# Optimization experiments

Measured on AMD Instinct MI355X. Metric: run time of the kernel, lower is better.

Reference implementation:

```python
import jax, jax.numpy as jnp
import numpy as np

N, E, F_IN, H, C = 50000, 800000, 64, 4, 32
NEG_SLOPE = 0.2  # PyG GATConv default negative_slope
LN_EPS = 1e-5


def setup_inputs() -> dict:
    key = jax.random.key(0)
    ks = jax.random.split(key, 8)
    s = 1.0 / np.sqrt(F_IN)
    return {
        "x": jax.random.normal(ks[0], (N, F_IN), jnp.float32),
        "edge_index": jax.random.randint(ks[1], (2, E), 0, N, jnp.int64),
        "W": jax.random.normal(ks[2], (F_IN, H * C), jnp.float32) * s,
        "att_src": jax.random.normal(ks[3], (H, C), jnp.float32) * s,
        "att_dst": jax.random.normal(ks[4], (H, C), jnp.float32) * s,
        "bias": jnp.zeros((H * C,), jnp.float32),
        "res_w": jax.random.normal(ks[5], (F_IN, H * C), jnp.float32) * s,
        "res_b": jnp.zeros((H * C,), jnp.float32),
        "ln_g": jnp.ones((H * C,), jnp.float32),
        "ln_b": jnp.zeros((H * C,), jnp.float32),
    }


def reference(x, edge_index, W, att_src, att_dst, bias, res_w, res_b, ln_g, ln_b):
    n = x.shape[0]
    # GATConv adds self-loops by default
    loop = jnp.arange(n, dtype=edge_index.dtype)
    src = jnp.concatenate([edge_index[0], loop])
    dst = jnp.concatenate([edge_index[1], loop])

    h = (x @ W).reshape(n, H, C)                      # [N,H,C]
    a_src = jnp.einsum('nhc,hc->nh', h, att_src)       # [N,H]
    a_dst = jnp.einsum('nhc,hc->nh', h, att_dst)

    e = a_src[src] + a_dst[dst]                        # [Etot,H]
    e = jnp.where(e >= 0, e, NEG_SLOPE * e)            # leaky_relu

    # segment softmax over destination nodes
    m = jax.ops.segment_max(e, dst, num_segments=n)    # [N,H]
    ex = jnp.exp(e - m[dst])
    denom = jax.ops.segment_sum(ex, dst, num_segments=n)
    alpha = ex / denom[dst]                            # [Etot,H]

    msg = h[src] * alpha[:, :, None]                   # [Etot,H,C]
    out = jax.ops.segment_sum(msg, dst, num_segments=n)  # [N,H,C]
    out = out.reshape(n, H * C) + bias

    # elu; dropout is identity in eval mode
    out = jnp.where(out > 0, out, jnp.expm1(out))
    out = out + (x @ res_w + res_b)                    # residual Linear

    mu = out.mean(-1, keepdims=True)
    var = ((out - mu) ** 2).mean(-1, keepdims=True)
    return ln_g * (out - mu) * jax.lax.rsqrt(var + LN_EPS) + ln_b
```

## Files before the change

### kernel.cpp

```cpp
#include <hip/hip_runtime.h>

#define F_IN 64
#define NH 4
#define HC 128
#define NEG_SLOPE 0.2f
#define LN_EPS 1e-5f
#define NC_CHUNK 128
#define BUCKET 128
#define KW_BLOCKS 64

typedef __bf16 bf16_8 __attribute__((ext_vector_type(8)));
typedef float  f32_4  __attribute__((ext_vector_type(4)));

__device__ inline int detect_is64(const int* __restrict__ ei, int E) {
    int lane = threadIdx.x & 63;
    long long stride = (2LL * E) / 65;
    int w = ei[(((long long)(lane + 1)) * stride) | 1];
    return __ballot(w != 0) == 0ULL;
}

__device__ inline unsigned bfpack(float a, float b) {
    unsigned ua = __float_as_uint(a), ub = __float_as_uint(b);
    ua = (ua + 0x7fffu + ((ua >> 16) & 1u)) >> 16;
    ub = (ub + 0x7fffu + ((ub >> 16) & 1u)) >> 16;
    return ua | (ub << 16);
}

__device__ inline float wave_bcast_sum(float v) {
#pragma unroll
    for (int off = 32; off > 0; off >>= 1) v += __shfl_down(v, off, 64);
    return __shfl(v, 0, 64);
}

__global__ __launch_bounds__(256) void k_prep(
    const float* __restrict__ W, const float* __restrict__ res_w,
    const int* __restrict__ ei, int E,
    __bf16* __restrict__ wt, int* __restrict__ counts, int NB, int chunk)
{
    if ((int)blockIdx.x < KW_BLOCKS) {
        int idx = blockIdx.x * 256 + threadIdx.x;
        int ch = idx >> 6, k = idx & 63;
        const float* src = (ch < HC) ? W : res_w;
        wt[ch * 64 + k] = (__bf16)src[k * HC + (ch & (HC - 1))];
        return;
    }
    __shared__ int cnt[512];
    int c = blockIdx.x - KW_BLOCKS;
    for (int i = threadIdx.x; i < NB; i += 256) cnt[i] = 0;
    __syncthreads();
    int is64 = detect_is64(ei, E);
    int base = c * chunk, end = min(E, base + chunk);
    for (int idx = base + threadIdx.x; idx < end; idx += 256) {
        int d = is64 ? ei[2 * (E + idx)] : ei[E + idx];
        atomicAdd(&cnt[d >> 7], 1);
    }
    __syncthreads();
    for (int b = threadIdx.x; b < NB; b += 256)
        counts[c * NB + b] = cnt[b];
}

__global__ __launch_bounds__(256) void k_main(
    const float* __restrict__ x, const __bf16* __restrict__ wt,
    const float* __restrict__ att_src, const float* __restrict__ att_dst,
    unsigned* __restrict__ h_bf, unsigned* __restrict__ r_bf,
    float* __restrict__ a_s, float* __restrict__ a_d, int n, int nka,
    const int* __restrict__ ei, int E, const int* __restrict__ counts,
    int* __restrict__ epacked, int* __restrict__ sbase_g, int NB, int chunk)
{
    __shared__ int cur[512];
    __shared__ int ss[256];

    if ((int)blockIdx.x < nka) {
        int tid = threadIdx.x;
        int wv_ = tid >> 6, lane = tid & 63;
        int col = lane & 15, quad = lane >> 4;
        int node = blockIdx.x * 64 + wv_ * 16 + col;
        int nrow = (node < n) ? node : (n - 1);

        bf16_8 bx0, bx1;
        {
            const float* xp = &x[nrow * F_IN + quad * 8];
            float4 p0 = *(const float4*)(xp);
            float4 p1 = *(const float4*)(xp + 4);
            float4 p2 = *(const float4*)(xp + 32);
            float4 p3 = *(const float4*)(xp + 36);
            bx0[0] = (__bf16)p0.x; bx0[1] = (__bf16)p0.y; bx0[2] = (__bf16)p0.z; bx0[3] = (__bf16)p0.w;
            bx0[4] = (__bf16)p1.x; bx0[5] = (__bf16)p1.y; bx0[6] = (__bf16)p1.z; bx0[7] = (__bf16)p1.w;
            bx1[0] = (__bf16)p2.x; bx1[1] = (__bf16)p2.y; bx1[2] = (__bf16)p2.z; bx1[3] = (__bf16)p2.w;
            bx1[4] = (__bf16)p3.x; bx1[5] = (__bf16)p3.y; bx1[6] = (__bf16)p3.z; bx1[7] = (__bf16)p3.w;
        }

        float vs[4] = {0.f, 0.f, 0.f, 0.f};
        float vd[4] = {0.f, 0.f, 0.f, 0.f};

#pragma unroll
        for (int mt = 0; mt < 16; ++mt) {
            const __bf16* ap = &wt[(mt * 16 + col) * 64 + quad * 8];
            bf16_8 a0 = *(const bf16_8*)ap;
            bf16_8 a1 = *(const bf16_8*)(ap + 32);
            f32_4 acc = {0.f, 0.f, 0.f, 0.f};
            acc = __builtin_amdgcn_mfma_f32_16x16x32_bf16(a0, bx0, acc, 0, 0, 0);
            acc = __builtin_amdgcn_mfma_f32_16x16x32_bf16(a1, bx1, acc, 0, 0, 0);
            int ch0 = mt * 16 + quad * 4;
            if (mt < 8) {
                float4 as4 = *(const float4*)&att_src[ch0];
                float4 ad4 = *(const float4*)&att_dst[ch0];
                int head = mt >> 1;
                vs[head] += acc[0] * as4.x + acc[1] * as4.y + acc[2] * as4.z + acc[3] * as4.w;
                vd[head] += acc[0] * ad4.x + acc[1] * ad4.y + acc[2] * ad4.z + acc[3] * ad4.w;
                if (node < n) {
                    uint2 pk = make_uint2(bfpack(acc[0], acc[1]), bfpack(acc[2], acc[3]));
                    *(uint2*)&h_bf[node * 64 + (ch0 >> 1)] = pk;
                }
            } else {
                if (node < n) {
                    uint2 pk = make_uint2(bfpack(acc[0], acc[1]), bfpack(acc[2], acc[3]));
                    *(uint2*)&r_bf[node * 64 + ((ch0 - 128) >> 1)] = pk;
                }
            }
        }

#pragma unroll
        for (int hh = 0; hh < NH; ++hh) {
            vs[hh] += __shfl_down(vs[hh], 32, 64);
            vs[hh] += __shfl_down(vs[hh], 16, 64);
            vd[hh] += __shfl_down(vd[hh], 32, 64);
            vd[hh] += __shfl_down(vd[hh], 16, 64);
        }
        if (quad == 0 && node < n) {
            *(float4*)&a_s[node * NH] = make_float4(vs[0], vs[1], vs[2], vs[3]);
            *(float4*)&a_d[node * NH] = make_float4(vd[0], vd[1], vd[2], vd[3]);
        }
        return;
    }

    int c = blockIdx.x - nka;
    int t = threadIdx.x;
    int b0 = 2 * t, b1 = 2 * t + 1;

    int f0 = 0, f1 = 0, p0 = 0, p1 = 0;
    for (int cc = 0; cc < NC_CHUNK; ++cc) {
        int v0 = (b0 < NB) ? counts[cc * NB + b0] : 0;
        int v1 = (b1 < NB) ? counts[cc * NB + b1] : 0;
        f0 += v0; f1 += v1;
        if (cc < c) { p0 += v0; p1 += v1; }
    }
    ss[t] = f0 + f1;
    __syncthreads();
#pragma unroll
    for (int off = 1; off < 256; off <<= 1) {
        int u = (t >= off) ? ss[t - off] : 0;
        __syncthreads();
        ss[t] += u;
        __syncthreads();
    }
    int ebase = ss[t] - (f0 + f1);
    int base0 = ebase;
    int base1 = ebase + f0;
    if (b0 < NB) cur[b0] = base0 + p0;
    if (b1 < NB) cur[b1] = base1 + p1;
    if (c == 0) {
        if (b0 <= NB) sbase_g[b0] = base0;
        if (b1 <= NB) sbase_g[b1] = base1;
    }
    __syncthreads();

    int is64 = detect_is64(ei, E);
    int base = c * chunk, end = min(E, base + chunk);
    for (int idx = base + t; idx < end; idx += 256) {
        int s = is64 ? ei[2 * idx] : ei[idx];
        int d = is64 ? ei[2 * (E + idx)] : ei[E + idx];
        int p = atomicAdd(&cur[d >> 7], 1);
        epacked[p] = ((d & (BUCKET - 1)) << 16) | s;
    }
}

__global__ __launch_bounds__(256) void kd_sort(
    const int* __restrict__ sbase_g, const int* __restrict__ epacked,
    int* __restrict__ sorted_src, int* __restrict__ offsets,
    int NB, int n, int E)
{
    __shared__ int hist[BUCKET];
    __shared__ int sc[BUCKET];
    __shared__ int cur[BUCKET];
    int b = blockIdx.x;
    int s0 = sbase_g[b];
    int s1 = sbase_g[b + 1];
    int t = threadIdx.x;
    if (t < BUCKET) hist[t] = 0;
    __syncthreads();
    for (int e = s0 + t; e < s1; e += 256)
        atomicAdd(&hist[((unsigned)epacked[e]) >> 16], 1);
    __syncthreads();
    if (t < BUCKET) sc[t] = hist[t];
    __syncthreads();
#pragma unroll
    for (int o = 1; o < BUCKET; o <<= 1) {
        int u = (t >= o && t < BUCKET) ? sc[t - o] : 0;
        __syncthreads();
        if (t < BUCKET) sc[t] += u;
        __syncthreads();
    }
    if (t < BUCKET) {
        int excl = sc[t] - hist[t];
        cur[t] = s0 + excl;
        int d = b * BUCKET + t;
        if (d < n) offsets[d] = s0 + excl;
    }
    if (b == NB - 1 && t == 0) offsets[n] = E;
    __syncthreads();
    for (int e = s0 + t; e < s1; e += 256) {
        int p = epacked[e];
        int pos = atomicAdd(&cur[((unsigned)p) >> 16], 1);
        sorted_src[pos] = p & 0xFFFF;
    }
}

__global__ __launch_bounds__(256) void k_agg(
    const int* __restrict__ offsets, const int* __restrict__ src_sorted,
    const float* __restrict__ a_s, const float* __restrict__ a_d,
    const unsigned int* __restrict__ h_bf, const unsigned int* __restrict__ r_bf,
    const float* __restrict__ bias, const float* __restrict__ res_b,
    const float* __restrict__ ln_g, const float* __restrict__ ln_b,
    float* __restrict__ out, int n)
{
    int wv = threadIdx.x >> 6, lane = threadIdx.x & 63;
    int d = blockIdx.x * 4 + wv;
    if (d >= n) return;
    int c0 = lane * 2, head = lane >> 4;
    float ad = a_d[d * NH + head];

    unsigned rv = r_bf[d * 64 + lane];
    float bi0 = bias[c0], bi1 = bias[c0 + 1];
    float rb0 = res_b[c0], rb1 = res_b[c0 + 1];
    float g0 = ln_g[c0], g1 = ln_g[c0 + 1];
    float lb0 = ln_b[c0], lb1 = ln_b[c0 + 1];

    float e = a_s[d * NH + head] + ad;
    e = (e >= 0.f) ? e : NEG_SLOPE * e;
    float w = __expf(e);
    float denom = w;
    unsigned hv = h_bf[d * 64 + lane];
    float ax = w * __uint_as_float(hv << 16);
    float ay = w * __uint_as_float(hv & 0xffff0000u);

    int lo = offsets[d], hi = offsets[d + 1];
    int k = lo;
    for (; k + 7 < hi; k += 8) {
        int s[8]; unsigned v[8]; float ee[8];
#pragma unroll
        for (int i = 0; i < 8; ++i) s[i] = src_sorted[k + i];
#pragma unroll
        for (int i = 0; i < 8; ++i) ee[i] = a_s[s[i] * NH + head];
#pragma unroll
        for (int i = 0; i < 8; ++i) v[i] = h_bf[s[i] * 64 + lane];
#pragma unroll
        for (int i = 0; i < 8; ++i) {
            float e0 = ee[i] + ad;
            e0 = (e0 >= 0.f) ? e0 : NEG_SLOPE * e0;
            float w0 = __expf(e0);
            denom += w0;
            ax += w0 * __uint_as_float(v[i] << 16);
            ay += w0 * __uint_as_float(v[i] & 0xffff0000u);
        }
    }
    for (; k < hi; ++k) {
        int s0 = src_sorted[k];
        float e0 = a_s[s0 * NH + head] + ad;
        unsigned v0 = h_bf[s0 * 64 + lane];
        e0 = (e0 >= 0.f) ? e0 : NEG_SLOPE * e0;
        float w0 = __expf(e0);
        denom += w0;
        ax += w0 * __uint_as_float(v0 << 16);
        ay += w0 * __uint_as_float(v0 & 0xffff0000u);
    }

    float inv = 1.f / denom;
    float ox = ax * inv + bi0;
    float oy = ay * inv + bi1;
    ox = (ox > 0.f) ? ox : expm1f(ox);
    oy = (oy > 0.f) ? oy : expm1f(oy);
    ox += __uint_as_float(rv << 16) + rb0;
    oy += __uint_as_float(rv & 0xffff0000u) + rb1;
    float mean = wave_bcast_sum(ox + oy) * (1.f / HC);
    float dx = ox - mean, dy = oy - mean;
    float var = wave_bcast_sum(dx * dx + dy * dy) * (1.f / HC);
    float rs = rsqrtf(var + LN_EPS);
    *(float2*)&out[d * HC + c0] =
        make_float2(g0 * dx * rs + lb0, g1 * dy * rs + lb1);
}

extern "C" void kernel_launch(void* const* d_in, const int* in_sizes, int n_in,
                              void* d_out, int out_size, void* d_ws, size_t ws_size,
                              hipStream_t stream) {
    const float* x       = (const float*)d_in[0];
    const int*   ei      = (const int*)d_in[1];
    const float* W       = (const float*)d_in[2];
    const float* att_src = (const float*)d_in[3];
    const float* att_dst = (const float*)d_in[4];
    const float* bias    = (const float*)d_in[5];
    const float* res_w   = (const float*)d_in[6];
    const float* res_b   = (const float*)d_in[7];
    const float* ln_g    = (const float*)d_in[8];
    const float* ln_b    = (const float*)d_in[9];
    float* out = (float*)d_out;

    int n = in_sizes[0] / F_IN;
    int E = in_sizes[1] / 2;
    int NB = (n + BUCKET - 1) / BUCKET;
    int chunk = (E + NC_CHUNK - 1) / NC_CHUNK;
    int nka = (n + 63) / 64;

    unsigned* h_bf     = (unsigned*)d_ws;
    unsigned* r_bf     = h_bf + (size_t)n * 64;
    float*    a_s      = (float*)(r_bf + (size_t)n * 64);
    float*    a_d      = a_s + (size_t)n * NH;
    int*      counts   = (int*)(a_d + (size_t)n * NH);
    int*      sbase_g  = counts + NC_CHUNK * NB;
    int*      epacked  = sbase_g + (NB + 2);
    int*      ssorted  = epacked + E;
    int*      offsets  = ssorted + E;
    __bf16*   wt       = (__bf16*)(offsets + (n + 2));

    k_prep<<<KW_BLOCKS + NC_CHUNK, 256, 0, stream>>>(
        W, res_w, ei, E, wt, counts, NB, chunk);

    k_main<<<nka + NC_CHUNK, 256, 0, stream>>>(
        x, wt, att_src, att_dst, h_bf, r_bf, a_s, a_d, n, nka,
        ei, E, counts, epacked, sbase_g, NB, chunk);

    kd_sort<<<NB, 256, 0, stream>>>(sbase_g, epacked, ssorted, offsets, NB, n, E);

    k_agg<<<(n + 3) / 4, 256, 0, stream>>>(offsets, ssorted, a_s, a_d, h_bf, r_bf,
                                           bias, res_b, ln_g, ln_b, out, n);
}
```

Baseline: 192.8 us.

## Split wave into two edge-halves in aggregation and double nodes per projection block

The aggregation kernel now splits each wave into two 32-lane halves. Each half handles alternate edges and loads 8 bytes of bf16 features per lane, and the halves are combined with xor shuffles before the ELU, residual and layernorm epilogue. Separately, the projection part of k_main processes two 16-node tiles per wave, so the weight fragments are reused across both and the block count halves. The first change aims to raise memory-level parallelism and access width in the gather loop, at the cost of extra shuffles and idle lanes in the epilogue store. The second cuts redundant weight loads but uses more registers per wave.

```diff
diff --git a/kernel.cpp b/kernel.cpp
--- a/kernel.cpp
+++ b/kernel.cpp
@@ -24,12 +24,6 @@
     ua = (ua + 0x7fffu + ((ua >> 16) & 1u)) >> 16;
     ub = (ub + 0x7fffu + ((ub >> 16) & 1u)) >> 16;
     return ua | (ub << 16);
-}
-
-__device__ inline float wave_bcast_sum(float v) {
-#pragma unroll
-    for (int off = 32; off > 0; off >>= 1) v += __shfl_down(v, off, 64);
-    return __shfl(v, 0, 64);
 }
 
 __global__ __launch_bounds__(256) void k_prep(
@@ -74,62 +68,95 @@
         int tid = threadIdx.x;
         int wv_ = tid >> 6, lane = tid & 63;
         int col = lane & 15, quad = lane >> 4;
-        int node = blockIdx.x * 64 + wv_ * 16 + col;
-        int nrow = (node < n) ? node : (n - 1);
-
-        bf16_8 bx0, bx1;
+        int base = blockIdx.x * 128;
+        int node0 = base + wv_ * 16 + col;
+        int node1 = node0 + 64;
+        int nr0 = (node0 < n) ? node0 : (n - 1);
+        int nr1 = (node1 < n) ? node1 : (n - 1);
+
+        bf16_8 b0x0, b0x1, b1x0, b1x1;
         {
-            const float* xp = &x[nrow * F_IN + quad * 8];
+            const float* xp = &x[nr0 * F_IN + quad * 8];
             float4 p0 = *(const float4*)(xp);
             float4 p1 = *(const float4*)(xp + 4);
             float4 p2 = *(const float4*)(xp + 32);
             float4 p3 = *(const float4*)(xp + 36);
-            bx0[0] = (__bf16)p0.x; bx0[1] = (__bf16)p0.y; bx0[2] = (__bf16)p0.z; bx0[3] = (__bf16)p0.w;
-            bx0[4] = (__bf16)p1.x; bx0[5] = (__bf16)p1.y; bx0[6] = (__bf16)p1.z; bx0[7] = (__bf16)p1.w;
-            bx1[0] = (__bf16)p2.x; bx1[1] = (__bf16)p2.y; bx1[2] = (__bf16)p2.z; bx1[3] = (__bf16)p2.w;
-            bx1[4] = (__bf16)p3.x; bx1[5] = (__bf16)p3.y; bx1[6] = (__bf16)p3.z; bx1[7] = (__bf16)p3.w;
-        }
-
-        float vs[4] = {0.f, 0.f, 0.f, 0.f};
-        float vd[4] = {0.f, 0.f, 0.f, 0.f};
+            b0x0[0] = (__bf16)p0.x; b0x0[1] = (__bf16)p0.y; b0x0[2] = (__bf16)p0.z; b0x0[3] = (__bf16)p0.w;
+            b0x0[4] = (__bf16)p1.x; b0x0[5] = (__bf16)p1.y; b0x0[6] = (__bf16)p1.z; b0x0[7] = (__bf16)p1.w;
+            b0x1[0] = (__bf16)p2.x; b0x1[1] = (__bf16)p2.y; b0x1[2] = (__bf16)p2.z; b0x1[3] = (__bf16)p2.w;
+            b0x1[4] = (__bf16)p3.x; b0x1[5] = (__bf16)p3.y; b0x1[6] = (__bf16)p3.z; b0x1[7] = (__bf16)p3.w;
+        }
+        {
+            const float* xp = &x[nr1 * F_IN + quad * 8];
+            float4 p0 = *(const float4*)(xp);
+            float4 p1 = *(const float4*)(xp + 4);
+            float4 p2 = *(const float4*)(xp + 32);
+            float4 p3 = *(const float4*)(xp + 36);
+            b1x0[0] = (__bf16)p0.x; b1x0[1] = (__bf16)p0.y; b1x0[2] = (__bf16)p0.z; b1x0[3] = (__bf16)p0.w;
+            b1x0[4] = (__bf16)p1.x; b1x0[5] = (__bf16)p1.y; b1x0[6] = (__bf16)p1.z; b1x0[7] = (__bf16)p1.w;
+            b1x1[0] = (__bf16)p2.x; b1x1[1] = (__bf16)p2.y; b1x1[2] = (__bf16)p2.z; b1x1[3] = (__bf16)p2.w;
+            b1x1[4] = (__bf16)p3.x; b1x1[5] = (__bf16)p3.y; b1x1[6] = (__bf16)p3.z; b1x1[7] = (__bf16)p3.w;
+        }
+
+        float vs0[4] = {0,0,0,0}, vd0[4] = {0,0,0,0};
+        float vs1[4] = {0,0,0,0}, vd1[4] = {0,0,0,0};
 
 #pragma unroll
         for (int mt = 0; mt < 16; ++mt) {
             const __bf16* ap = &wt[(mt * 16 + col) * 64 + quad * 8];
             bf16_8 a0 = *(const bf16_8*)ap;
             bf16_8 a1 = *(const bf16_8*)(ap + 32);
-            f32_4 acc = {0.f, 0.f, 0.f, 0.f};
-            acc = __builtin_amdgcn_mfma_f32_16x16x32_bf16(a0, bx0, acc, 0, 0, 0);
-            acc = __builtin_amdgcn_mfma_f32_16x16x32_bf16(a1, bx1, acc, 0, 0, 0);
+            f32_4 acc0 = {0.f, 0.f, 0.f, 0.f};
+            acc0 = __builtin_amdgcn_mfma_f32_16x16x32_bf16(a0, b0x0, acc0, 0, 0, 0);
+            acc0 = __builtin_amdgcn_mfma_f32_16x16x32_bf16(a1, b0x1, acc0, 0, 0, 0);
+            f32_4 acc1 = {0.f, 0.f, 0.f, 0.f};
+            acc1 = __builtin_amdgcn_mfma_f32_16x16x32_bf16(a0, b1x0, acc1, 0, 0, 0);
+            acc1 = __builtin_amdgcn_mfma_f32_16x16x32_bf16(a1, b1x1, acc1, 0, 0, 0);
             int ch0 = mt * 16 + quad * 4;
             if (mt < 8) {
                 float4 as4 = *(const float4*)&att_src[ch0];
                 float4 ad4 = *(const float4*)&att_dst[ch0];
                 int head = mt >> 1;
-                vs[head] += acc[0] * as4.x + acc[1] * as4.y + acc[2] * as4.z + acc[3] * as4.w;
-                vd[head] += acc[0] * ad4.x + acc[1] * ad4.y + acc[2] * ad4.z + acc[3] * ad4.w;
-                if (node < n) {
-                    uint2 pk = make_uint2(bfpack(acc[0], acc[1]), bfpack(acc[2], acc[3]));
-                    *(uint2*)&h_bf[node * 64 + (ch0 >> 1)] = pk;
+                vs0[head] += acc0[0]*as4.x + acc0[1]*as4.y + acc0[2]*as4.z + acc0[3]*as4.w;
+                vd0[head] += acc0[0]*ad4.x + acc0[1]*ad4.y + acc0[2]*ad4.z + acc0[3]*ad4.w;
+                vs1[head] += acc1[0]*as4.x + acc1[1]*as4.y + acc1[2]*as4.z + acc1[3]*as4.w;
+                vd1[head] += acc1[0]*ad4.x + acc1[1]*ad4.y + acc1[2]*ad4.z + acc1[3]*ad4.w;
+                if (node0 < n) {
+                    uint2 pk = make_uint2(bfpack(acc0[0], acc0[1]), bfpack(acc0[2], acc0[3]));
+                    *(uint2*)&h_bf[node0 * 64 + (ch0 >> 1)] = pk;
+                }
+                if (node1 < n) {
+                    uint2 pk = make_uint2(bfpack(acc1[0], acc1[1]), bfpack(acc1[2], acc1[3]));
+                    *(uint2*)&h_bf[node1 * 64 + (ch0 >> 1)] = pk;
                 }
             } else {
-                if (node < n) {
-                    uint2 pk = make_uint2(bfpack(acc[0], acc[1]), bfpack(acc[2], acc[3]));
-                    *(uint2*)&r_bf[node * 64 + ((ch0 - 128) >> 1)] = pk;
+                if (node0 < n) {
+                    uint2 pk = make_uint2(bfpack(acc0[0], acc0[1]), bfpack(acc0[2], acc0[3]));
+                    *(uint2*)&r_bf[node0 * 64 + ((ch0 - 128) >> 1)] = pk;
+                }
+                if (node1 < n) {
+                    uint2 pk = make_uint2(bfpack(acc1[0], acc1[1]), bfpack(acc1[2], acc1[3]));
+                    *(uint2*)&r_bf[node1 * 64 + ((ch0 - 128) >> 1)] = pk;
                 }
             }
         }
 
 #pragma unroll
         for (int hh = 0; hh < NH; ++hh) {
-            vs[hh] += __shfl_down(vs[hh], 32, 64);
-            vs[hh] += __shfl_down(vs[hh], 16, 64);
-            vd[hh] += __shfl_down(vd[hh], 32, 64);
-            vd[hh] += __shfl_down(vd[hh], 16, 64);
-        }
-        if (quad == 0 && node < n) {
-            *(float4*)&a_s[node * NH] = make_float4(vs[0], vs[1], vs[2], vs[3]);
-            *(float4*)&a_d[node * NH] = make_float4(vd[0], vd[1], vd[2], vd[3]);
+            vs0[hh] += __shfl_down(vs0[hh], 32, 64); vs0[hh] += __shfl_down(vs0[hh], 16, 64);
+            vd0[hh] += __shfl_down(vd0[hh], 32, 64); vd0[hh] += __shfl_down(vd0[hh], 16, 64);
+            vs1[hh] += __shfl_down(vs1[hh], 32, 64); vs1[hh] += __shfl_down(vs1[hh], 16, 64);
+            vd1[hh] += __shfl_down(vd1[hh], 32, 64); vd1[hh] += __shfl_down(vd1[hh], 16, 64);
+        }
+        if (quad == 0) {
+            if (node0 < n) {
+                *(float4*)&a_s[node0 * NH] = make_float4(vs0[0], vs0[1], vs0[2], vs0[3]);
+                *(float4*)&a_d[node0 * NH] = make_float4(vd0[0], vd0[1], vd0[2], vd0[3]);
+            }
+            if (node1 < n) {
+                *(float4*)&a_s[node1 * NH] = make_float4(vs1[0], vs1[1], vs1[2], vs1[3]);
+                *(float4*)&a_d[node1 * NH] = make_float4(vd1[0], vd1[1], vd1[2], vd1[3]);
+            }
         }
         return;
     }
@@ -155,8 +182,7 @@
         __syncthreads();
     }
     int ebase = ss[t] - (f0 + f1);
-    int base0 = ebase;
-    int base1 = ebase + f0;
+    int base0 = ebase, base1 = ebase + f0;
     if (b0 < NB) cur[b0] = base0 + p0;
     if (b1 < NB) cur[b1] = base1 + p1;
     if (c == 0) {
@@ -227,67 +253,103 @@
     int wv = threadIdx.x >> 6, lane = threadIdx.x & 63;
     int d = blockIdx.x * 4 + wv;
     if (d >= n) return;
-    int c0 = lane * 2, head = lane >> 4;
+    int eh = lane >> 5, g = lane & 31;
+    int head = g >> 3;
     float ad = a_d[d * NH + head];
 
-    unsigned rv = r_bf[d * 64 + lane];
-    float bi0 = bias[c0], bi1 = bias[c0 + 1];
-    float rb0 = res_b[c0], rb1 = res_b[c0 + 1];
-    float g0 = ln_g[c0], g1 = ln_g[c0 + 1];
-    float lb0 = ln_b[c0], lb1 = ln_b[c0 + 1];
-
-    float e = a_s[d * NH + head] + ad;
-    e = (e >= 0.f) ? e : NEG_SLOPE * e;
-    float w = __expf(e);
-    float denom = w;
-    unsigned hv = h_bf[d * 64 + lane];
-    float ax = w * __uint_as_float(hv << 16);
-    float ay = w * __uint_as_float(hv & 0xffff0000u);
+    float a0 = 0.f, a1 = 0.f, a2 = 0.f, a3 = 0.f, denom = 0.f;
+
+    {
+        float e = a_s[d * NH + head] + ad;
+        e = (e >= 0.f) ? e : NEG_SLOPE * e;
+        float w = (eh == 0) ? __expf(e) : 0.f;
+        uint2 hv = *(const uint2*)&h_bf[d * 64 + 2 * g];
+        a0 += w * __uint_as_float(hv.x << 16);
+        a1 += w * __uint_as_float(hv.x & 0xffff0000u);
+        a2 += w * __uint_as_float(hv.y << 16);
+        a3 += w * __uint_as_float(hv.y & 0xffff0000u);
+        denom += w;
+    }
 
     int lo = offsets[d], hi = offsets[d + 1];
     int k = lo;
     for (; k + 7 < hi; k += 8) {
-        int s[8]; unsigned v[8]; float ee[8];
-#pragma unroll
-        for (int i = 0; i < 8; ++i) s[i] = src_sorted[k + i];
-#pragma unroll
-        for (int i = 0; i < 8; ++i) ee[i] = a_s[s[i] * NH + head];
-#pragma unroll
-        for (int i = 0; i < 8; ++i) v[i] = h_bf[s[i] * 64 + lane];
-#pragma unroll
-        for (int i = 0; i < 8; ++i) {
+        int s[4]; float ee[4]; uint2 v[4];
+#pragma unroll
+        for (int i = 0; i < 4; ++i) s[i] = src_sorted[k + 2 * i + eh];
+#pragma unroll
+        for (int i = 0; i < 4; ++i) ee[i] = a_s[s[i] * NH + head];
+#pragma unroll
+        for (int i = 0; i < 4; ++i) v[i] = *(const uint2*)&h_bf[s[i] * 64 + 2 * g];
+#pragma unroll
+        for (int i = 0; i < 4; ++i) {
             float e0 = ee[i] + ad;
             e0 = (e0 >= 0.f) ? e0 : NEG_SLOPE * e0;
             float w0 = __expf(e0);
             denom += w0;
-            ax += w0 * __uint_as_float(v[i] << 16);
-            ay += w0 * __uint_as_float(v[i] & 0xffff0000u);
-        }
-    }
-    for (; k < hi; ++k) {
-        int s0 = src_sorted[k];
+            a0 += w0 * __uint_as_float(v[i].x << 16);
+            a1 += w0 * __uint_as_float(v[i].x & 0xffff0000u);
+            a2 += w0 * __uint_as_float(v[i].y << 16);
+            a3 += w0 * __uint_as_float(v[i].y & 0xffff0000u);
+        }
+    }
+    for (; k < hi; k += 2) {
+        int idx = k + eh;
+        int valid = idx < hi;
+        int s0 = valid ? src_sorted[idx] : 0;
         float e0 = a_s[s0 * NH + head] + ad;
-        unsigned v0 = h_bf[s0 * 64 + lane];
+        uint2 v0 = *(const uint2*)&h_bf[s0 * 64 + 2 * g];
         e0 = (e0 >= 0.f) ? e0 : NEG_SLOPE * e0;
-        float w0 = __expf(e0);
+        float w0 = valid ? __expf(e0) : 0.f;
         denom += w0;
-        ax += w0 * __uint_as_float(v0 << 16);
-        ay += w0 * __uint_as_float(v0 & 0xffff0000u);
-    }
+        a0 += w0 * __uint_as_float(v0.x << 16);
+        a1 += w0 * __uint_as_float(v0.x & 0xffff0000u);
+        a2 += w0 * __uint_as_float(v0.y << 16);
+        a3 += w0 * __uint_as_float(v0.y & 0xffff0000u);
+    }
+
+    a0 += __shfl_xor(a0, 32, 64);
+    a1 += __shfl_xor(a1, 32, 64);
+    a2 += __shfl_xor(a2, 32, 64);
+    a3 += __shfl_xor(a3, 32, 64);
+    denom += __shfl_xor(denom, 32, 64);
+
+    int c0 = g * 4;
+    float4 bi = *(const float4*)&bias[c0];
+    float4 rb = *(const float4*)&res_b[c0];
+    float4 gg = *(const float4*)&ln_g[c0];
+    float4 lb = *(const float4*)&ln_b[c0];
+    uint2 rv = *(const uint2*)&r_bf[d * 64 + 2 * g];
 
     float inv = 1.f / denom;
-    float ox = ax * inv + bi0;
-    float oy = ay * inv + bi1;
-    ox = (ox > 0.f) ? ox : expm1f(ox);
-    oy = (oy > 0.f) ? oy : expm1f(oy);
-    ox += __uint_as_float(rv << 16) + rb0;
-    oy += __uint_as_float(rv & 0xffff0000u) + rb1;
-    float mean = wave_bcast_sum(ox + oy) * (1.f / HC);
-    float dx = ox - mean, dy = oy - mean;
-    float var = wave_bcast_sum(dx * dx + dy * dy) * (1.f / HC);
+    float o0 = a0 * inv + bi.x;
+    float o1 = a1 * inv + bi.y;
+    float o2 = a2 * inv + bi.z;
+    float o3 = a3 * inv + bi.w;
+    o0 = (o0 > 0.f) ? o0 : expm1f(o0);
+    o1 = (o1 > 0.f) ? o1 : expm1f(o1);
+    o2 = (o2 > 0.f) ? o2 : expm1f(o2);
+    o3 = (o3 > 0.f) ? o3 : expm1f(o3);
+    o0 += __uint_as_float(rv.x << 16) + rb.x;
+    o1 += __uint_as_float(rv.x & 0xffff0000u) + rb.y;
+    o2 += __uint_as_float(rv.y << 16) + rb.z;
+    o3 += __uint_as_float(rv.y & 0xffff0000u) + rb.w;
+
+    float ps = o0 + o1 + o2 + o3;
+#pragma unroll
+    for (int off = 32; off > 0; off >>= 1) ps += __shfl_down(ps, off, 64);
+    float mean = __shfl(ps, 0, 64) * (1.f / (2 * HC));
+    float d0 = o0 - mean, d1 = o1 - mean, d2 = o2 - mean, d3 = o3 - mean;
+    float pv = d0 * d0 + d1 * d1 + d2 * d2 + d3 * d3;
+#pragma unroll
+    for (int off = 32; off > 0; off >>= 1) pv += __shfl_down(pv, off, 64);
+    float var = __shfl(pv, 0, 64) * (1.f / (2 * HC));
     float rs = rsqrtf(var + LN_EPS);
-    *(float2*)&out[d * HC + c0] =
-        make_float2(g0 * dx * rs + lb0, g1 * dy * rs + lb1);
+    if (eh == 0) {
+        *(float4*)&out[d * HC + c0] =
+            make_float4(gg.x * d0 * rs + lb.x, gg.y * d1 * rs + lb.y,
+                        gg.z * d2 * rs + lb.z, gg.w * d3 * rs + lb.w);
+    }
 }
 
 extern "C" void kernel_launch(void* const* d_in, const int* in_sizes, int n_in,
@@ -309,7 +371,7 @@
     int E = in_sizes[1] / 2;
     int NB = (n + BUCKET - 1) / BUCKET;
     int chunk = (E + NC_CHUNK - 1) / NC_CHUNK;
-    int nka = (n + 63) / 64;
+    int nka = (n + 127) / 128;
 
     unsigned* h_bf     = (unsigned*)d_ws;
     unsigned* r_bf     = h_bf + (size_t)n * 64;
```

Measured after the change: 189.3 us. No clear change (-1.8%).

## Split aggregation wave into four edge groups with 16-byte row loads

Applied to the files above, without the earlier changes.

The aggregation kernel now splits each wave into four 16-lane groups. Each group handles a different edge and loads 8 bf16 channels per lane as one uint4, where before each lane loaded a single 4-byte word for all 64 lanes per edge. Partial sums are combined with xor shuffles before the ELU, residual and LayerNorm epilogue. This puts more independent gathers in flight with wider memory accesses, at the cost of more registers, duplicated epilogue work and masked tail handling. The edge-sort chunk count is also doubled to 256.

```diff
diff --git a/kernel.cpp b/kernel.cpp
--- a/kernel.cpp
+++ b/kernel.cpp
@@ -5,7 +5,7 @@
 #define HC 128
 #define NEG_SLOPE 0.2f
 #define LN_EPS 1e-5f
-#define NC_CHUNK 128
+#define NC_CHUNK 256
 #define BUCKET 128
 #define KW_BLOCKS 64
 
@@ -24,12 +24,6 @@
     ua = (ua + 0x7fffu + ((ua >> 16) & 1u)) >> 16;
     ub = (ub + 0x7fffu + ((ub >> 16) & 1u)) >> 16;
     return ua | (ub << 16);
-}
-
-__device__ inline float wave_bcast_sum(float v) {
-#pragma unroll
-    for (int off = 32; off > 0; off >>= 1) v += __shfl_down(v, off, 64);
-    return __shfl(v, 0, 64);
 }
 
 __global__ __launch_bounds__(256) void k_prep(
@@ -155,8 +149,7 @@
         __syncthreads();
     }
     int ebase = ss[t] - (f0 + f1);
-    int base0 = ebase;
-    int base1 = ebase + f0;
+    int base0 = ebase, base1 = ebase + f0;
     if (b0 < NB) cur[b0] = base0 + p0;
     if (b1 < NB) cur[b1] = base1 + p1;
     if (c == 0) {
@@ -227,67 +220,132 @@
     int wv = threadIdx.x >> 6, lane = threadIdx.x & 63;
     int d = blockIdx.x * 4 + wv;
     if (d >= n) return;
-    int c0 = lane * 2, head = lane >> 4;
+    int eq = lane >> 4, g = lane & 15;
+    int head = g >> 2;
     float ad = a_d[d * NH + head];
 
-    unsigned rv = r_bf[d * 64 + lane];
-    float bi0 = bias[c0], bi1 = bias[c0 + 1];
-    float rb0 = res_b[c0], rb1 = res_b[c0 + 1];
-    float g0 = ln_g[c0], g1 = ln_g[c0 + 1];
-    float lb0 = ln_b[c0], lb1 = ln_b[c0 + 1];
-
-    float e = a_s[d * NH + head] + ad;
-    e = (e >= 0.f) ? e : NEG_SLOPE * e;
-    float w = __expf(e);
-    float denom = w;
-    unsigned hv = h_bf[d * 64 + lane];
-    float ax = w * __uint_as_float(hv << 16);
-    float ay = w * __uint_as_float(hv & 0xffff0000u);
+    float a0 = 0.f, a1 = 0.f, a2 = 0.f, a3 = 0.f;
+    float a4 = 0.f, a5 = 0.f, a6 = 0.f, a7 = 0.f, denom = 0.f;
+
+    {
+        float e = a_s[d * NH + head] + ad;
+        e = (e >= 0.f) ? e : NEG_SLOPE * e;
+        float w = (eq == 0) ? __expf(e) : 0.f;
+        uint4 hv = *(const uint4*)&h_bf[d * 64 + g * 4];
+        a0 += w * __uint_as_float(hv.x << 16);
+        a1 += w * __uint_as_float(hv.x & 0xffff0000u);
+        a2 += w * __uint_as_float(hv.y << 16);
+        a3 += w * __uint_as_float(hv.y & 0xffff0000u);
+        a4 += w * __uint_as_float(hv.z << 16);
+        a5 += w * __uint_as_float(hv.z & 0xffff0000u);
+        a6 += w * __uint_as_float(hv.w << 16);
+        a7 += w * __uint_as_float(hv.w & 0xffff0000u);
+        denom += w;
+    }
 
     int lo = offsets[d], hi = offsets[d + 1];
     int k = lo;
     for (; k + 7 < hi; k += 8) {
-        int s[8]; unsigned v[8]; float ee[8];
-#pragma unroll
-        for (int i = 0; i < 8; ++i) s[i] = src_sorted[k + i];
-#pragma unroll
-        for (int i = 0; i < 8; ++i) ee[i] = a_s[s[i] * NH + head];
-#pragma unroll
-        for (int i = 0; i < 8; ++i) v[i] = h_bf[s[i] * 64 + lane];
-#pragma unroll
-        for (int i = 0; i < 8; ++i) {
+        int s[2]; float ee[2]; uint4 v[2];
+#pragma unroll
+        for (int i = 0; i < 2; ++i) s[i] = src_sorted[k + 4 * i + eq];
+#pragma unroll
+        for (int i = 0; i < 2; ++i) ee[i] = a_s[s[i] * NH + head];
+#pragma unroll
+        for (int i = 0; i < 2; ++i) v[i] = *(const uint4*)&h_bf[s[i] * 64 + g * 4];
+#pragma unroll
+        for (int i = 0; i < 2; ++i) {
             float e0 = ee[i] + ad;
             e0 = (e0 >= 0.f) ? e0 : NEG_SLOPE * e0;
             float w0 = __expf(e0);
             denom += w0;
-            ax += w0 * __uint_as_float(v[i] << 16);
-            ay += w0 * __uint_as_float(v[i] & 0xffff0000u);
-        }
-    }
-    for (; k < hi; ++k) {
-        int s0 = src_sorted[k];
+            a0 += w0 * __uint_as_float(v[i].x << 16);
+            a1 += w0 * __uint_as_float(v[i].x & 0xffff0000u);
+            a2 += w0 * __uint_as_float(v[i].y << 16);
+            a3 += w0 * __uint_as_float(v[i].y & 0xffff0000u);
+            a4 += w0 * __uint_as_float(v[i].z << 16);
+            a5 += w0 * __uint_as_float(v[i].z & 0xffff0000u);
+            a6 += w0 * __uint_as_float(v[i].w << 16);
+            a7 += w0 * __uint_as_float(v[i].w & 0xffff0000u);
+        }
+    }
+    for (; k < hi; k += 4) {
+        int idx = k + eq;
+        int valid = idx < hi;
+        int s0 = valid ? src_sorted[idx] : 0;
         float e0 = a_s[s0 * NH + head] + ad;
-        unsigned v0 = h_bf[s0 * 64 + lane];
+        uint4 v0 = *(const uint4*)&h_bf[s0 * 64 + g * 4];
         e0 = (e0 >= 0.f) ? e0 : NEG_SLOPE * e0;
-        float w0 = __expf(e0);
+        float w0 = valid ? __expf(e0) : 0.f;
         denom += w0;
-        ax += w0 * __uint_as_float(v0 << 16);
-        ay += w0 * __uint_as_float(v0 & 0xffff0000u);
-    }
+        a0 += w0 * __uint_as_float(v0.x << 16);
+        a1 += w0 * __uint_as_float(v0.x & 0xffff0000u);
+        a2 += w0 * __uint_as_float(v0.y << 16);
+        a3 += w0 * __uint_as_float(v0.y & 0xffff0000u);
+        a4 += w0 * __uint_as_float(v0.z << 16);
+        a5 += w0 * __uint_as_float(v0.z & 0xffff0000u);
+        a6 += w0 * __uint_as_float(v0.w << 16);
+        a7 += w0 * __uint_as_float(v0.w & 0xffff0000u);
+    }
+
+    a0 += __shfl_xor(a0, 16, 64); a0 += __shfl_xor(a0, 32, 64);
+    a1 += __shfl_xor(a1, 16, 64); a1 += __shfl_xor(a1, 32, 64);
+    a2 += __shfl_xor(a2, 16, 64); a2 += __shfl_xor(a2, 32, 64);
+    a3 += __shfl_xor(a3, 16, 64); a3 += __shfl_xor(a3, 32, 64);
+    a4 += __shfl_xor(a4, 16, 64); a4 += __shfl_xor(a4, 32, 64);
+    a5 += __shfl_xor(a5, 16, 64); a5 += __shfl_xor(a5, 32, 64);
+    a6 += __shfl_xor(a6, 16, 64); a6 += __shfl_xor(a6, 32, 64);
+    a7 += __shfl_xor(a7, 16, 64); a7 += __shfl_xor(a7, 32, 64);
+    denom += __shfl_xor(denom, 16, 64); denom += __shfl_xor(denom, 32, 64);
+
+    int c0 = g * 8;
+    float4 biA = *(const float4*)&bias[c0],  biB = *(const float4*)&bias[c0 + 4];
+    float4 rbA = *(const float4*)&res_b[c0], rbB = *(const float4*)&res_b[c0 + 4];
+    float4 ggA = *(const float4*)&ln_g[c0],  ggB = *(const float4*)&ln_g[c0 + 4];
+    float4 lbA = *(const float4*)&ln_b[c0],  lbB = *(const float4*)&ln_b[c0 + 4];
+    uint4 rv = *(const uint4*)&r_bf[d * 64 + g * 4];
 
     float inv = 1.f / denom;
-    float ox = ax * inv + bi0;
-    float oy = ay * inv + bi1;
-    ox = (ox > 0.f) ? ox : expm1f(ox);
-    oy = (oy > 0.f) ? oy : expm1f(oy);
-    ox += __uint_as_float(rv << 16) + rb0;
-    oy += __uint_as_float(rv & 0xffff0000u) + rb1;
-    float mean = wave_bcast_sum(ox + oy) * (1.f / HC);
-    float dx = ox - mean, dy = oy - mean;
-    float var = wave_bcast_sum(dx * dx + dy * dy) * (1.f / HC);
+    float o0 = a0 * inv + biA.x, o1 = a1 * inv + biA.y;
+    float o2 = a2 * inv + biA.z, o3 = a3 * inv + biA.w;
+    float o4 = a4 * inv + biB.x, o5 = a5 * inv + biB.y;
+    float o6 = a6 * inv + biB.z, o7 = a7 * inv + biB.w;
+    o0 = (o0 > 0.f) ? o0 : expm1f(o0);
+    o1 = (o1 > 0.f) ? o1 : expm1f(o1);
+    o2 = (o2 > 0.f) ? o2 : expm1f(o2);
+    o3 = (o3 > 0.f) ? o3 : expm1f(o3);
+    o4 = (o4 > 0.f) ? o4 : expm1f(o4);
+    o5 = (o5 > 0.f) ? o5 : expm1f(o5);
+    o6 = (o6 > 0.f) ? o6 : expm1f(o6);
+    o7 = (o7 > 0.f) ? o7 : expm1f(o7);
+    o0 += __uint_as_float(rv.x << 16) + rbA.x;
+    o1 += __uint_as_float(rv.x & 0xffff0000u) + rbA.y;
+    o2 += __uint_as_float(rv.y << 16) + rbA.z;
+    o3 += __uint_as_float(rv.y & 0xffff0000u) + rbA.w;
+    o4 += __uint_as_float(rv.z << 16) + rbB.x;
+    o5 += __uint_as_float(rv.z & 0xffff0000u) + rbB.y;
+    o6 += __uint_as_float(rv.w << 16) + rbB.z;
+    o7 += __uint_as_float(rv.w & 0xffff0000u) + rbB.w;
+
+    float ps = ((o0 + o1) + (o2 + o3)) + ((o4 + o5) + (o6 + o7));
+#pragma unroll
+    for (int off = 32; off > 0; off >>= 1) ps += __shfl_down(ps, off, 64);
+    float mean = __shfl(ps, 0, 64) * (1.f / (4 * HC));
+    float d0 = o0 - mean, d1 = o1 - mean, d2 = o2 - mean, d3 = o3 - mean;
+    float d4 = o4 - mean, d5 = o5 - mean, d6 = o6 - mean, d7 = o7 - mean;
+    float pv = ((d0*d0 + d1*d1) + (d2*d2 + d3*d3)) + ((d4*d4 + d5*d5) + (d6*d6 + d7*d7));
+#pragma unroll
+    for (int off = 32; off > 0; off >>= 1) pv += __shfl_down(pv, off, 64);
+    float var = __shfl(pv, 0, 64) * (1.f / (4 * HC));
     float rs = rsqrtf(var + LN_EPS);
-    *(float2*)&out[d * HC + c0] =
-        make_float2(g0 * dx * rs + lb0, g1 * dy * rs + lb1);
+    if (eq == 0) {
+        *(float4*)&out[d * HC + c0] =
+            make_float4(ggA.x * d0 * rs + lbA.x, ggA.y * d1 * rs + lbA.y,
+                        ggA.z * d2 * rs + lbA.z, ggA.w * d3 * rs + lbA.w);
+        *(float4*)&out[d * HC + c0 + 4] =
+            make_float4(ggB.x * d4 * rs + lbB.x, ggB.y * d5 * rs + lbB.y,
+                        ggB.z * d6 * rs + lbB.z, ggB.w * d7 * rs + lbB.w);
+    }
 }
 
 extern "C" void kernel_launch(void* const* d_in, const int* in_sizes, int n_in,
```

Result: slower. 205.7 us (+6.7%).
